# Kernel optimization log

Hardware: AMD Instinct MI355X
Metric: run time of the kernel (lower is better)

The kernel has to match this reference:

```python
import jax, jax.numpy as jnp
import numpy as np

B, DIM, N = 64, 128, 4000
H = 4
DH = DIM // H          # 32
CL = 50                # clusters (hardcoded in module)
K = 9                  # knn_num
SCALOR = DH ** -0.5


def setup_inputs() -> dict:
    key = jax.random.key(0)
    ks = jax.random.split(key, 16)
    s = 0.05
    inp = {
        'x': jax.random.normal(ks[0], (B, DIM, N, 1), jnp.float32),
        # conv_group1 / conv_group2: InstanceNorm(no affine) -> BN(affine) -> ReLU -> 1x1 conv
        'wg1': jax.random.normal(ks[1], (CL, DIM), jnp.float32) * s,
        'bg1': jnp.zeros((CL,), jnp.float32),
        'g1_gamma': jnp.ones((DIM,), jnp.float32),
        'g1_beta': jnp.zeros((DIM,), jnp.float32),
        'wg2': jax.random.normal(ks[2], (CL, DIM), jnp.float32) * s,
        'bg2': jnp.zeros((CL,), jnp.float32),
        'g2_gamma': jnp.ones((DIM,), jnp.float32),
        'g2_beta': jnp.zeros((DIM,), jnp.float32),
        # per-head 1x1 convs (stacked over heads)
        'qkv_w': jax.random.normal(ks[3], (H, DH, DIM), jnp.float32) * s,
        'qkv_b': jnp.zeros((H, DH), jnp.float32),
        'qkv1_w': jax.random.normal(ks[4], (H, 3 * DH, DIM), jnp.float32) * s,
        'qkv1_b': jnp.zeros((H, 3 * DH), jnp.float32),
        # GCBlock convs: conv1 (1,3) stride (1,3): 2*DH->DH ; conv2 (1,3): DH->DH
        'gc1_w': jax.random.normal(ks[5], (H, DH, 2 * DH, 3), jnp.float32) * s,
        'gc1_b': jnp.zeros((H, DH), jnp.float32),
        'gc1_gamma': jnp.ones((H, DH), jnp.float32),
        'gc1_beta': jnp.zeros((H, DH), jnp.float32),
        'gc2_w': jax.random.normal(ks[6], (H, DH, DH, 3), jnp.float32) * s,
        'gc2_b': jnp.zeros((H, DH), jnp.float32),
        'gc2_gamma': jnp.ones((H, DH), jnp.float32),
        'gc2_beta': jnp.zeros((H, DH), jnp.float32),
        # output projections
        'pres_w': jax.random.normal(ks[7], (DIM, 2 * DIM), jnp.float32) * s,
        'pres_b': jnp.zeros((DIM,), jnp.float32),
        'proj_w': jax.random.normal(ks[8], (DIM, DIM), jnp.float32) * s,
        'proj_b': jnp.zeros((DIM,), jnp.float32),
    }
    return inp


def _conv_group(x3, w, bconv, gamma, beta):
    # x3: (b, C, n). InstanceNorm2d(eps=1e-3, no affine) over n, BN(train) over (b,n), ReLU, 1x1 conv.
    mu = x3.mean(-1, keepdims=True)
    var = x3.var(-1, keepdims=True)
    xin = (x3 - mu) * jax.lax.rsqrt(var + 1e-3)
    mu2 = xin.mean((0, 2), keepdims=True)
    var2 = xin.var((0, 2), keepdims=True)
    xbn = gamma[None, :, None] * (xin - mu2) * jax.lax.rsqrt(var2 + 1e-5) + beta[None, :, None]
    xr = jax.nn.relu(xbn)
    return jnp.einsum('oc,bcn->bon', w, xr) + bconv[None, :, None]


def _bn_train(h, gamma, beta, axes):
    mu = h.mean(axes, keepdims=True)
    var = h.var(axes, keepdims=True)
    return gamma * (h - mu) * jax.lax.rsqrt(var + 1e-5) + beta


def _forward(x, wg1, bg1, g1_gamma, g1_beta, wg2, bg2, g2_gamma, g2_beta,
             qkv_w, qkv_b, qkv1_w, qkv1_b,
             gc1_w, gc1_b, gc1_gamma, gc1_beta,
             gc2_w, gc2_b, gc2_gamma, gc2_beta,
             pres_w, pres_b, proj_w, proj_b):
    xs = x[..., 0]                                          # (b, dim, n)
    # cluster assignment 1: softmax over points
    embed1 = _conv_group(xs, wg1, bg1, g1_gamma, g1_beta)   # (b, 50, n)
    S1 = jax.nn.softmax(embed1, axis=2)
    cluster_x = jnp.einsum('bdn,bcn->bdc', xs, S1)          # (b, dim, 50)

    # ---- local branch (per head, vectorized): 1x1 conv -> knn graph feature -> conv stack ----
    q = jnp.einsum('hod,bdc->bhoc', qkv_w, cluster_x) + qkv_b[None, :, :, None]  # (b,H,dh,50)
    xt = q.transpose(0, 1, 3, 2)                            # (b,H,50,dh)
    inner = jnp.einsum('bhnc,bhmc->bhnm', xt, xt)
    sq = jnp.sum(xt * xt, axis=-1)
    pd = 2.0 * inner - sq[..., :, None] - sq[..., None, :]  # negative squared distance
    idx = jax.lax.top_k(pd, K)[1]                            # (b,H,50,K)
    x_exp = jnp.broadcast_to(xt[:, :, None, :, :], xt.shape[:2] + (CL, CL, DH))
    feature = jnp.take_along_axis(x_exp, idx[..., None], axis=3)        # (b,H,50,K,dh)
    center = jnp.broadcast_to(xt[:, :, :, None, :], feature.shape)
    edge = jnp.concatenate([center, center - feature], axis=-1)          # (b,H,50,K,2dh)
    # conv1: kernel (1,3) stride (1,3): K=9 -> 3 windows of 3
    e = edge.reshape(edge.shape[0], H, CL, 3, 3, 2 * DH)
    h1 = jnp.einsum('bhnjti,hoit->bhnjo', e, gc1_w) + gc1_b[None, :, None, None, :]
    h1 = jax.nn.relu(_bn_train(h1, gc1_gamma[None, :, None, None, :], gc1_beta[None, :, None, None, :], (0, 2, 3)))
    # conv2: kernel (1,3): 3 -> 1
    h2 = jnp.einsum('bhnti,hoit->bhno', h1, gc2_w) + gc2_b[None, :, None, :]
    h2 = jax.nn.relu(_bn_train(h2, gc2_gamma[None, :, None, :], gc2_beta[None, :, None, :], (0, 2)))
    local = h2.transpose(0, 1, 3, 2)                        # (b,H,dh,50)

    # ---- global branch: tiny attention over 50 clusters per head ----
    qkv = jnp.einsum('hod,bdc->bhoc', qkv1_w, cluster_x) + qkv1_b[None, :, :, None]  # (b,H,3dh,50)
    qg, kg, vg = jnp.split(qkv, 3, axis=2)
    attn = jax.nn.softmax(SCALOR * jnp.einsum('bhdn,bhdm->bhnm', qg, kg), axis=-1)
    glob = jnp.einsum('bhnm,bhdm->bhdn', attn, vg)          # (b,H,dh,50)

    # interleave [local_h, global_h] per head along channels -> (b, 2*dim, 50)
    per_head = jnp.concatenate([local, glob], axis=2)       # (b,H,2dh,50)
    cat = per_head.reshape(per_head.shape[0], 2 * DIM, CL)
    res = jnp.einsum('oc,bcn->bon', pres_w, cat) + pres_b[None, :, None]  # (b,dim,50)

    # cluster assignment 2: softmax over clusters, scatter back to points
    embed2 = _conv_group(xs, wg2, bg2, g2_gamma, g2_beta)   # (b,50,n)
    S2 = jax.nn.softmax(embed2, axis=1)
    res2 = jnp.einsum('bdc,bcn->bdn', res, S2)              # (b,dim,n)
    out = jnp.einsum('od,bdn->bon', proj_w, res2) + proj_b[None, :, None]
    return out[..., None]                                   # (b,dim,n,1)


def reference(x, wg1, bg1, g1_gamma, g1_beta, wg2, bg2, g2_gamma, g2_beta,
              qkv_w, qkv_b, qkv1_w, qkv1_b,
              gc1_w, gc1_b, gc1_gamma, gc1_beta,
              gc2_w, gc2_b, gc2_gamma, gc2_beta,
              pres_w, pres_b, proj_w, proj_b):
    return _forward(x, wg1, bg1, g1_gamma, g1_beta, wg2, bg2, g2_gamma, g2_beta,
                    qkv_w, qkv_b, qkv1_w, qkv1_b,
                    gc1_w, gc1_b, gc1_gamma, gc1_beta,
                    gc2_w, gc2_b, gc2_gamma, gc2_beta,
                    pres_w, pres_b, proj_w, proj_b)
```

## Files before the change

kernel.cpp:

```cpp
#include <hip/hip_runtime.h>
#include <cstddef>


constexpr size_t O_MU    = 0;
constexpr size_t O_RINV  = 8192;
constexpr size_t O_RATIO = 16384;
constexpr size_t O_A1    = 24576;
constexpr size_t O_B1    = 24704;
constexpr size_t O_A2    = 24832;
constexpr size_t O_B2    = 24960;
constexpr size_t O_PROJWT= 25088;
constexpr size_t O_VPROJ = 41472;
constexpr size_t O_MT    = 41600;
constexpr size_t O_E2    = 74368;
constexpr size_t O_UCXP  = 12874368;
constexpr size_t O_CX    = 16659072;
constexpr size_t O_XT    = 17068672;
constexpr size_t O_QT    = 17478272;
constexpr size_t O_KT    = 17887872;
constexpr size_t O_VT    = 18297472;
constexpr size_t O_H1    = 18707072;
constexpr size_t O_P1    = 19935872;
constexpr size_t O_BN1S  = 19952256;
constexpr size_t O_BN1T  = 19952384;
constexpr size_t O_H2    = 19952512;
constexpr size_t O_P2    = 20362112;
constexpr size_t O_BN2S  = 20378496;
constexpr size_t O_BN2T  = 20378624;
constexpr size_t O_CAT   = 20378752;
constexpr size_t O_PRES2 = 21197952;

__global__ __launch_bounds__(256) void k_rowstats(const float* __restrict__ x,
                                                  float* __restrict__ ws){
  int row = blockIdx.x;
  const float4* xr = (const float4*)(x + (size_t)row * 4000);
  float s = 0.f, sq = 0.f;
  for(int i = threadIdx.x; i < 1000; i += 256){
    float4 v = xr[i];
    s  += v.x + v.y + v.z + v.w;
    sq += v.x*v.x + v.y*v.y + v.z*v.z + v.w*v.w;
  }
  __shared__ float ls[256], lq[256];
  ls[threadIdx.x] = s; lq[threadIdx.x] = sq; __syncthreads();
  for(int st = 128; st > 0; st >>= 1){
    if(threadIdx.x < st){ ls[threadIdx.x] += ls[threadIdx.x+st]; lq[threadIdx.x] += lq[threadIdx.x+st]; }
    __syncthreads();
  }
  if(threadIdx.x == 0){
    float mean = ls[0] * (1.f/4000.f);
    float var  = lq[0] * (1.f/4000.f) - mean*mean;
    ws[O_MU   + row] = mean;
    ws[O_RINV + row] = rsqrtf(var + 1e-3f);
    ws[O_RATIO+ row] = var / (var + 1e-3f);
  }
}

__global__ void k_prep(const float* g1g, const float* g1b,
                       const float* g2g, const float* g2b,
                       const float* presb, const float* projw,
                       float* __restrict__ ws){
  int t = threadIdx.x;
  if(t < 128){
    float s = 0.f;
    for(int b = 0; b < 64; b++) s += ws[O_RATIO + b*128 + t];
    float var2 = s * (1.f/64.f);
    float inv2 = rsqrtf(var2 + 1e-5f);
    ws[O_A1+t] = g1g[t] * inv2;  ws[O_B1+t] = g1b[t];
    ws[O_A2+t] = g2g[t] * inv2;  ws[O_B2+t] = g2b[t];
  }
  for(int i = t; i < 16384; i += 256){ int o = i & 127, k = i >> 7; ws[O_PROJWT+i] = projw[o*128 + k]; }
  __syncthreads();
  if(t < 128){
    float v = 0.f;
    for(int d = 0; d < 128; d++) v += ws[O_PROJWT + d*128 + t] * presb[d];
    ws[O_VPROJ + t] = v;
  }
}

__global__ __launch_bounds__(256) void k_mprep(const float* __restrict__ presw,
                                               float* __restrict__ ws){
  int kk2 = blockIdx.x * 2;
  __shared__ float pwc[2][128];
  int t = threadIdx.x;
  { int which = t >> 7, d = t & 127; pwc[which][d] = presw[d*256 + kk2 + which]; }
  __syncthreads();
  int which = t >> 7, o = t & 127;
  float acc = 0.f;
  for(int d = 0; d < 128; d++) acc += ws[O_PROJWT + d*128 + o] * pwc[which][d];
  ws[O_MT + (size_t)(kk2 + which)*128 + o] = acc;
}

__global__ __launch_bounds__(256) void k_e1ucx(const float* __restrict__ x,
    const float* __restrict__ wg1, const float* __restrict__ bg1,
    float* __restrict__ ws){
  int ch = blockIdx.x, b = blockIdx.y;
  __shared__ float lW1[128*52];
  __shared__ float lrv1[128*48];
  __shared__ float lxt [48*132];
  __shared__ float ca1[128], cb1[128];
  __shared__ float bg1p[56];
  int t = threadIdx.x;
  if(t < 128){
    float mu = ws[O_MU + b*128 + t], ri = ws[O_RINV + b*128 + t];
    float a1 = ws[O_A1+t]*ri;
    ca1[t] = a1; cb1[t] = ws[O_B1+t] - a1*mu;
  }
  if(t < 56) bg1p[t] = (t < 50) ? bg1[t] : 0.f;
  for(int i = t; i < 1664; i += 256){
    int cl = i >> 5, cq = i & 31;
    float4 w = (cl < 50) ? *(const float4*)&wg1[cl*128 + cq*4] : make_float4(0.f,0.f,0.f,0.f);
    int c0 = cq*4;
    lW1[(c0+0)*52+cl] = w.x; lW1[(c0+1)*52+cl] = w.y;
    lW1[(c0+2)*52+cl] = w.z; lW1[(c0+3)*52+cl] = w.w;
  }
  int dg = t & 31, cg = t >> 5;
  float ua[4][8];
  #pragma unroll
  for(int r = 0; r < 4; r++)
    #pragma unroll
    for(int i = 0; i < 8; i++) ua[r][i] = 0.f;
  float zacc = 0.f;
  int ig = t >> 4, jg = t & 15;
  int clb = ig*4, j4 = jg*4;

  for(int st = 0; st < 11; st++){
    int nb = ch*500 + st*48;
    int lim = (st == 10) ? 20 : 48;
    __syncthreads();
    for(int i = t; i < 1536; i += 256){
      int c = i / 12, jj = (i % 12)*4;
      float4 xv = make_float4(0.f,0.f,0.f,0.f);
      if(jj < lim) xv = *(const float4*)&x[(size_t)(b*128 + c)*4000 + nb + jj];
      lxt[(jj+0)*132 + c] = xv.x; lxt[(jj+1)*132 + c] = xv.y;
      lxt[(jj+2)*132 + c] = xv.z; lxt[(jj+3)*132 + c] = xv.w;
      float a1 = ca1[c], b1v = cb1[c];
      float4 r1;
      r1.x = fmaxf(a1*xv.x + b1v, 0.f); r1.y = fmaxf(a1*xv.y + b1v, 0.f);
      r1.z = fmaxf(a1*xv.z + b1v, 0.f); r1.w = fmaxf(a1*xv.w + b1v, 0.f);
      *(float4*)&lrv1[c*48 + jj] = r1;
    }
    __syncthreads();
    float e[4][4];
    if(ig < 13 && jg < 12){
      #pragma unroll
      for(int r = 0; r < 4; r++){ e[r][0]=0.f; e[r][1]=0.f; e[r][2]=0.f; e[r][3]=0.f; }
      #pragma unroll 4
      for(int c = 0; c < 128; c++){
        float4 w = *(const float4*)&lW1[c*52 + clb];
        float4 v = *(const float4*)&lrv1[c*48 + j4];
        e[0][0] += w.x*v.x; e[0][1] += w.x*v.y; e[0][2] += w.x*v.z; e[0][3] += w.x*v.w;
        e[1][0] += w.y*v.x; e[1][1] += w.y*v.y; e[1][2] += w.y*v.z; e[1][3] += w.y*v.w;
        e[2][0] += w.z*v.x; e[2][1] += w.z*v.y; e[2][2] += w.z*v.z; e[2][3] += w.z*v.w;
        e[3][0] += w.w*v.x; e[3][1] += w.w*v.y; e[3][2] += w.w*v.z; e[3][3] += w.w*v.w;
      }
    }
    __syncthreads();
    if(ig < 13 && jg < 12){
      bool live = (j4 < lim);
      #pragma unroll
      for(int r = 0; r < 4; r++){
        float bias = bg1p[clb + r];
        float4 u = make_float4(0.f,0.f,0.f,0.f);
        if(live){
          u.x = expf(e[r][0] + bias); u.y = expf(e[r][1] + bias);
          u.z = expf(e[r][2] + bias); u.w = expf(e[r][3] + bias);
        }
        *(float4*)&lrv1[(clb + r)*48 + j4] = u;
      }
    }
    __syncthreads();
    if(t < 224){
      int d4 = dg*4, c8 = cg*8;
      for(int n4 = 0; n4 < 12; n4++){
        int n0 = n4*4;
        float4 uv[8];
        #pragma unroll
        for(int i = 0; i < 8; i++) uv[i] = *(const float4*)&lrv1[(c8 + i)*48 + n0];
        {
          float4 xq = *(const float4*)&lxt[(n0+0)*132 + d4];
          #pragma unroll
          for(int i = 0; i < 8; i++){
            float u = uv[i].x;
            ua[0][i] += xq.x*u; ua[1][i] += xq.y*u; ua[2][i] += xq.z*u; ua[3][i] += xq.w*u;
          }
        }
        {
          float4 xq = *(const float4*)&lxt[(n0+1)*132 + d4];
          #pragma unroll
          for(int i = 0; i < 8; i++){
            float u = uv[i].y;
            ua[0][i] += xq.x*u; ua[1][i] += xq.y*u; ua[2][i] += xq.z*u; ua[3][i] += xq.w*u;
          }
        }
        {
          float4 xq = *(const float4*)&lxt[(n0+2)*132 + d4];
          #pragma unroll
          for(int i = 0; i < 8; i++){
            float u = uv[i].z;
            ua[0][i] += xq.x*u; ua[1][i] += xq.y*u; ua[2][i] += xq.z*u; ua[3][i] += xq.w*u;
          }
        }
        {
          float4 xq = *(const float4*)&lxt[(n0+3)*132 + d4];
          #pragma unroll
          for(int i = 0; i < 8; i++){
            float u = uv[i].w;
            ua[0][i] += xq.x*u; ua[1][i] += xq.y*u; ua[2][i] += xq.z*u; ua[3][i] += xq.w*u;
          }
        }
      }
    }
    if(t < 52){
      float s = 0.f;
      #pragma unroll
      for(int k = 0; k < 12; k++){
        float4 u = *(const float4*)&lrv1[t*48 + k*4];
        s += u.x + u.y + u.z + u.w;
      }
      zacc += s;
    }
  }
  if(t < 224){
    int d4 = dg*4, c8 = cg*8;
    #pragma unroll
    for(int r = 0; r < 4; r++){
      size_t base = O_UCXP + ((size_t)(ch*64 + b)*132 + d4 + r)*56 + c8;
      *(float4*)&ws[base]     = make_float4(ua[r][0], ua[r][1], ua[r][2], ua[r][3]);
      *(float4*)&ws[base + 4] = make_float4(ua[r][4], ua[r][5], ua[r][6], ua[r][7]);
    }
  }
  if(t < 52) ws[O_UCXP + ((size_t)(ch*64 + b)*132 + 128)*56 + t] = zacc;
}

__global__ __launch_bounds__(256) void k_e2(const float* __restrict__ x,
    const float* __restrict__ wg2, const float* __restrict__ bg2,
    float* __restrict__ ws){
  int ch = blockIdx.x, b = blockIdx.y;
  __shared__ float lW2[128*52];
  __shared__ float lrv2[128*64];
  __shared__ float ca2[128], cb2[128];
  __shared__ float bg2p[56];
  int t = threadIdx.x;
  if(t < 128){
    float mu = ws[O_MU + b*128 + t], ri = ws[O_RINV + b*128 + t];
    float a2 = ws[O_A2+t]*ri;
    ca2[t] = a2; cb2[t] = ws[O_B2+t] - a2*mu;
  }
  if(t < 56) bg2p[t] = (t < 50) ? bg2[t] : 0.f;
  for(int i = t; i < 1664; i += 256){
    int cl = i >> 5, cq = i & 31;
    float4 w = (cl < 50) ? *(const float4*)&wg2[cl*128 + cq*4] : make_float4(0.f,0.f,0.f,0.f);
    int c0 = cq*4;
    lW2[(c0+0)*52+cl] = w.x; lW2[(c0+1)*52+cl] = w.y;
    lW2[(c0+2)*52+cl] = w.z; lW2[(c0+3)*52+cl] = w.w;
  }
  int ig = t >> 4, jg = t & 15;
  int clb = ig*4, j4 = jg*4;
  for(int st = 0; st < 8; st++){
    int nb = ch*500 + st*64;
    int lim = (st == 7) ? 52 : 64;
    __syncthreads();
    for(int i = t; i < 2048; i += 256){
      int c = i >> 4, jj = (i & 15)*4;
      float4 xv = make_float4(0.f,0.f,0.f,0.f);
      if(jj < lim) xv = *(const float4*)&x[(size_t)(b*128 + c)*4000 + nb + jj];
      float a2 = ca2[c], b2v = cb2[c];
      float4 r2;
      r2.x = fmaxf(a2*xv.x + b2v, 0.f); r2.y = fmaxf(a2*xv.y + b2v, 0.f);
      r2.z = fmaxf(a2*xv.z + b2v, 0.f); r2.w = fmaxf(a2*xv.w + b2v, 0.f);
      *(float4*)&lrv2[c*64 + jj] = r2;
    }
    __syncthreads();
    if(ig < 13){
      float e[4][4];
      #pragma unroll
      for(int r = 0; r < 4; r++){ e[r][0]=0.f; e[r][1]=0.f; e[r][2]=0.f; e[r][3]=0.f; }
      #pragma unroll 4
      for(int c = 0; c < 128; c++){
        float4 w = *(const float4*)&lW2[c*52 + clb];
        float4 v = *(const float4*)&lrv2[c*64 + j4];
        e[0][0] += w.x*v.x; e[0][1] += w.x*v.y; e[0][2] += w.x*v.z; e[0][3] += w.x*v.w;
        e[1][0] += w.y*v.x; e[1][1] += w.y*v.y; e[1][2] += w.y*v.z; e[1][3] += w.y*v.w;
        e[2][0] += w.z*v.x; e[2][1] += w.z*v.y; e[2][2] += w.z*v.z; e[2][3] += w.z*v.w;
        e[3][0] += w.w*v.x; e[3][1] += w.w*v.y; e[3][2] += w.w*v.z; e[3][3] += w.w*v.w;
      }
      if(j4 < lim){
        #pragma unroll
        for(int r = 0; r < 4; r++){
          int cl = clb + r;
          if(cl < 50){
            float bias = bg2p[cl];
            float4 o = make_float4(e[r][0]+bias, e[r][1]+bias, e[r][2]+bias, e[r][3]+bias);
            *(float4*)&ws[O_E2 + ((size_t)b*50 + cl)*4000 + nb + j4] = o;
          }
        }
      }
    }
  }
}

__global__ __launch_bounds__(256) void k_cxred(float* __restrict__ ws){
  int b = blockIdx.x, t = threadIdx.x;
  __shared__ float zi[64];
  if(t < 50){
    float s = 0.f;
    for(int ch = 0; ch < 8; ch++)
      s += ws[O_UCXP + ((size_t)(ch*64 + b)*132 + 128)*56 + t];
    zi[t] = 1.f / s;
  }
  __syncthreads();
  for(int i = t; i < 6400; i += 256){
    int d = i / 50, c = i % 50;
    float s = 0.f;
    for(int ch = 0; ch < 8; ch++)
      s += ws[O_UCXP + ((size_t)(ch*64 + b)*132 + d)*56 + c];
    ws[O_CX + (size_t)b*6400 + d*50 + c] = s * zi[c];
  }
}

__global__ __launch_bounds__(256) void k_qkv(const float* __restrict__ qw,
                                             const float* __restrict__ qb,
                                             const float* __restrict__ q1w,
                                             const float* __restrict__ q1b,
                                             float* __restrict__ ws){
  int rt = blockIdx.x, b = blockIdx.y;
  __shared__ float wl[64*130];
  __shared__ float cxl[128*52];
  int t = threadIdx.x;
  for(int i = t; i < 2048; i += 256){
    int rl = i >> 5, kq = i & 31, row = rt*64 + rl;
    float4 w = (row < 128) ? *(const float4*)&qw[row*128 + kq*4]
                           : *(const float4*)&q1w[(row-128)*128 + kq*4];
    int k0 = kq*4;
    wl[rl*130 + k0+0] = w.x; wl[rl*130 + k0+1] = w.y;
    wl[rl*130 + k0+2] = w.z; wl[rl*130 + k0+3] = w.w;
  }
  for(int i = t; i < 6656; i += 256){
    int k = i / 52, c = i % 52;
    cxl[i] = (c < 50) ? ws[O_CX + (size_t)b*6400 + k*50 + c] : 0.f;
  }
  __syncthreads();
  int ig = t & 15, cg = t >> 4;
  float acc[4][4];
  #pragma unroll
  for(int r = 0; r < 4; r++){ acc[r][0]=0.f; acc[r][1]=0.f; acc[r][2]=0.f; acc[r][3]=0.f; }
  if(cg < 13){
    int rb = ig*4, cb = cg*4;
    #pragma unroll 4
    for(int k = 0; k < 128; k++){
      float4 cv = *(const float4*)&cxl[k*52 + cb];
      float w0 = wl[(rb+0)*130 + k], w1 = wl[(rb+1)*130 + k];
      float w2 = wl[(rb+2)*130 + k], w3 = wl[(rb+3)*130 + k];
      acc[0][0] += w0*cv.x; acc[0][1] += w0*cv.y; acc[0][2] += w0*cv.z; acc[0][3] += w0*cv.w;
      acc[1][0] += w1*cv.x; acc[1][1] += w1*cv.y; acc[1][2] += w1*cv.z; acc[1][3] += w1*cv.w;
      acc[2][0] += w2*cv.x; acc[2][1] += w2*cv.y; acc[2][2] += w2*cv.z; acc[2][3] += w2*cv.w;
      acc[3][0] += w3*cv.x; acc[3][1] += w3*cv.y; acc[3][2] += w3*cv.z; acc[3][3] += w3*cv.w;
    }
    #pragma unroll
    for(int r = 0; r < 4; r++){
      int row = rt*64 + ig*4 + r;
      size_t base; float bias;
      if(row < 128){
        int h = row >> 5;
        bias = qb[row];
        base = O_XT + (size_t)(b*4 + h)*1600 + (row & 31);
      }else{
        int r2 = row - 128, h = r2/96, j = r2%96, kind = j >> 5, dd = j & 31;
        bias = q1b[r2];
        base = (kind==0 ? O_QT : kind==1 ? O_KT : O_VT) + (size_t)(b*4 + h)*1600 + dd;
      }
      #pragma unroll
      for(int s = 0; s < 4; s++){
        int c = cg*4 + s;
        if(c < 50) ws[base + (size_t)c*32] = acc[r][s] + bias;
      }
    }
  }
}

__global__ __launch_bounds__(256) void k_knn(const float* __restrict__ g1w,
                                             const float* __restrict__ g1bias,
                                             float* __restrict__ ws){
  int h = blockIdx.x, b = blockIdx.y;
  __shared__ float xtl[50][33];
  __shared__ float pdl[50][52];
  __shared__ float sql[50];
  __shared__ int   idxl[50][9];
  __shared__ float w1l[6144];
  int t = threadIdx.x;
  const float* xtg = ws + O_XT + (size_t)(b*4 + h)*1600;
  for(int i = t; i < 1600; i += 256) xtl[i >> 5][i & 31] = xtg[i];
  for(int i = t; i < 6144; i += 256){
    int o = i / 192, r = i % 192, ii = r / 3, tt = r % 3;
    w1l[(ii*3 + tt)*32 + o] = g1w[(size_t)h*6144 + i];
  }
  __syncthreads();
  if(t < 50){
    float s = 0.f;
    for(int d = 0; d < 32; d++){ float v = xtl[t][d]; s += v*v; }
    sql[t] = s;
  }
  __syncthreads();
  for(int i = t; i < 2500; i += 256){
    int n = i / 50, m = i % 50;
    float s = 0.f;
    for(int d = 0; d < 32; d++) s += xtl[n][d]*xtl[m][d];
    pdl[n][m] = 2.f*s - sql[n] - sql[m];
  }
  __syncthreads();
  if(t < 50){
    float pv = INFINITY; int pi = -1;
    for(int k = 0; k < 9; k++){
      float bv = -INFINITY; int bi = 1000;
      for(int m = 0; m < 50; m++){
        float v = pdl[t][m];
        bool elig = (v < pv) || (v == pv && m > pi);
        if(elig && (v > bv || (v == bv && m < bi))){ bv = v; bi = m; }
      }
      idxl[t][k] = bi; pv = bv; pi = bi;
    }
  }
  __syncthreads();
  if(t < 150){
    int n = t / 3, jw = t % 3;
    float acc[32];
    #pragma unroll
    for(int o = 0; o < 32; o++) acc[o] = 0.f;
    for(int t3 = 0; t3 < 3; t3++){
      int kx = idxl[n][jw*3 + t3];
      for(int ii = 0; ii < 32; ii++){
        float c0 = xtl[n][ii];
        float c1 = c0 - xtl[kx][ii];
        const float* wr0 = w1l + (ii*3 + t3)*32;
        const float* wr1 = w1l + ((ii+32)*3 + t3)*32;
        #pragma unroll
        for(int o = 0; o < 32; o++) acc[o] += c0*wr0[o] + c1*wr1[o];
      }
    }
    float* out = ws + O_H1 + ((size_t)(b*4 + h)*150 + n*3 + jw)*32;
    #pragma unroll
    for(int o = 0; o < 32; o++) out[o] = acc[o] + g1bias[h*32 + o];
  }
}

__global__ void k_bn1p(float* __restrict__ ws){
  int b = blockIdx.x, t = threadIdx.x;
  int p = t & 127, half = t >> 7;
  int h = p >> 5, o = p & 31;
  const float* src = ws + O_H1 + (size_t)b*19200;
  float s = 0.f, sq = 0.f;
  for(int nj = half*75; nj < half*75 + 75; nj++){
    float v = src[(h*150 + nj)*32 + o];
    s += v; sq += v*v;
  }
  __shared__ float ls[256], lq[256];
  ls[t] = s; lq[t] = sq; __syncthreads();
  if(t < 128){
    ws[O_P1 + b*256 + p]       = ls[t] + ls[t+128];
    ws[O_P1 + b*256 + 128 + p] = lq[t] + lq[t+128];
  }
}

__global__ void k_bn1f(const float* g, const float* be, float* __restrict__ ws){
  int t = threadIdx.x;
  if(t < 128){
    float s = 0.f, sq = 0.f;
    for(int b = 0; b < 64; b++){ s += ws[O_P1 + b*256 + t]; sq += ws[O_P1 + b*256 + 128 + t]; }
    float mean = s * (1.f/9600.f), var = sq * (1.f/9600.f) - mean*mean;
    float sc = g[t] * rsqrtf(var + 1e-5f);
    ws[O_BN1S+t] = sc; ws[O_BN1T+t] = be[t] - sc*mean;
  }
}

__global__ __launch_bounds__(256) void k_conv2(const float* __restrict__ g2w,
                                               const float* __restrict__ g2bias,
                                               float* __restrict__ ws){
  int h = blockIdx.x, b = blockIdx.y;
  __shared__ float hl[150][33];
  __shared__ float w2l[3072];
  __shared__ float rs[8][32], rq[8][32];
  int t = threadIdx.x;
  const float* h1p = ws + O_H1 + (size_t)(b*4 + h)*4800;
  for(int i = t; i < 4800; i += 256){
    int nj = i >> 5, ii = i & 31;
    hl[nj][ii] = fmaxf(ws[O_BN1S + h*32 + ii]*h1p[i] + ws[O_BN1T + h*32 + ii], 0.f);
  }
  for(int i = t; i < 3072; i += 256){
    int o = i / 96, r = i % 96, ii = r / 3, tt = r % 3;
    w2l[(ii*3 + tt)*32 + o] = g2w[(size_t)h*3072 + i];
  }
  __syncthreads();
  int o = t & 31, ng = t >> 5;
  float bias = g2bias[h*32 + o];
  float s = 0.f, sq = 0.f;
  for(int n = ng; n < 50; n += 8){
    float acc = 0.f;
    for(int t3 = 0; t3 < 3; t3++){
      const float* hr = hl[n*3 + t3];
      #pragma unroll
      for(int ii = 0; ii < 32; ii++) acc += hr[ii] * w2l[(ii*3 + t3)*32 + o];
    }
    acc += bias;
    ws[O_H2 + ((size_t)(b*4 + h)*50 + n)*32 + o] = acc;
    s += acc; sq += acc*acc;
  }
  rs[ng][o] = s; rq[ng][o] = sq; __syncthreads();
  if(t < 32){
    float S = 0.f, Q = 0.f;
    for(int g2 = 0; g2 < 8; g2++){ S += rs[g2][t]; Q += rq[g2][t]; }
    ws[O_P2 + (b*4 + h)*64 + t]      = S;
    ws[O_P2 + (b*4 + h)*64 + 32 + t] = Q;
  }
}

__global__ void k_bn2f(const float* g, const float* be, float* __restrict__ ws){
  int t = threadIdx.x;
  if(t < 128){
    int h = t >> 5, o = t & 31;
    float s = 0.f, sq = 0.f;
    for(int b = 0; b < 64; b++){
      s  += ws[O_P2 + (size_t)(b*4 + h)*64 + o];
      sq += ws[O_P2 + (size_t)(b*4 + h)*64 + 32 + o];
    }
    float mean = s * (1.f/3200.f), var = sq * (1.f/3200.f) - mean*mean;
    float sc = g[t] * rsqrtf(var + 1e-5f);
    ws[O_BN2S+t] = sc; ws[O_BN2T+t] = be[t] - sc*mean;
  }
}

__global__ __launch_bounds__(256) void k_attn(float* __restrict__ ws){
  int h = blockIdx.x, b = blockIdx.y;
  __shared__ float qtl[50][33], ktl[50][33], vtl[50][33], al[50][52];
  int t = threadIdx.x;
  size_t base = (size_t)(b*4 + h)*1600;
  for(int i = t; i < 1600; i += 256){
    int n = i >> 5, d = i & 31;
    qtl[n][d] = ws[O_QT + base + i];
    ktl[n][d] = ws[O_KT + base + i];
    vtl[n][d] = ws[O_VT + base + i];
  }
  __syncthreads();
  for(int i = t; i < 2500; i += 256){
    int n = i / 50, m = i % 50;
    float s = 0.f;
    for(int d = 0; d < 32; d++) s += qtl[n][d]*ktl[m][d];
    al[n][m] = s * 0.17677669529663687f;
  }
  __syncthreads();
  if(t < 50){
    float m = -INFINITY;
    for(int j = 0; j < 50; j++) m = fmaxf(m, al[t][j]);
    float s = 0.f;
    for(int j = 0; j < 50; j++){ float e = expf(al[t][j] - m); al[t][j] = e; s += e; }
    float inv = 1.f/s;
    for(int j = 0; j < 50; j++) al[t][j] *= inv;
  }
  __syncthreads();
  for(int i = t; i < 1600; i += 256){
    int n = i >> 5, d = i & 31;
    float gacc = 0.f;
    for(int m = 0; m < 50; m++) gacc += al[n][m]*vtl[m][d];
    ws[O_CAT + ((size_t)b*256 + h*64 + 32 + d)*50 + n] = gacc;
    float l = fmaxf(ws[O_BN2S + h*32 + d]*ws[O_H2 + ((size_t)(b*4 + h)*50 + n)*32 + d] + ws[O_BN2T + h*32 + d], 0.f);
    ws[O_CAT + ((size_t)b*256 + h*64 + d)*50 + n] = l;
  }
}

__global__ __launch_bounds__(256) void k_res(float* __restrict__ ws){
  int b = blockIdx.x;
  __shared__ float mtl[64*132];
  __shared__ float catl[64*52];
  __shared__ float vp[128];
  int t = threadIdx.x;
  if(t < 128) vp[t] = ws[O_VPROJ + t];
  int og = t >> 4, cg = t & 15;
  int ob = og*8, cb = cg*4;
  float acc[8][4];
  #pragma unroll
  for(int r = 0; r < 8; r++){ acc[r][0]=0.f; acc[r][1]=0.f; acc[r][2]=0.f; acc[r][3]=0.f; }
  for(int kc = 0; kc < 4; kc++){
    int k0 = kc*64;
    __syncthreads();
    for(int i = t; i < 2048; i += 256){
      int k = i >> 5, oq = i & 31;
      float4 m = *(const float4*)&ws[O_MT + (size_t)(k0 + k)*128 + oq*4];
      *(float4*)&mtl[k*132 + oq*4] = m;
    }
    for(int i = t; i < 3328; i += 256){
      int k = i / 52, c = i % 52;
      catl[i] = (c < 50) ? ws[O_CAT + (size_t)b*12800 + (k0 + k)*50 + c] : 0.f;
    }
    __syncthreads();
    if(cg < 13){
      #pragma unroll 2
      for(int k = 0; k < 64; k++){
        float4 m0 = *(const float4*)&mtl[k*132 + ob];
        float4 m1 = *(const float4*)&mtl[k*132 + ob + 4];
        float4 cv = *(const float4*)&catl[k*52 + cb];
        acc[0][0] += m0.x*cv.x; acc[0][1] += m0.x*cv.y; acc[0][2] += m0.x*cv.z; acc[0][3] += m0.x*cv.w;
        acc[1][0] += m0.y*cv.x; acc[1][1] += m0.y*cv.y; acc[1][2] += m0.y*cv.z; acc[1][3] += m0.y*cv.w;
        acc[2][0] += m0.z*cv.x; acc[2][1] += m0.z*cv.y; acc[2][2] += m0.z*cv.z; acc[2][3] += m0.z*cv.w;
        acc[3][0] += m0.w*cv.x; acc[3][1] += m0.w*cv.y; acc[3][2] += m0.w*cv.z; acc[3][3] += m0.w*cv.w;
        acc[4][0] += m1.x*cv.x; acc[4][1] += m1.x*cv.y; acc[4][2] += m1.x*cv.z; acc[4][3] += m1.x*cv.w;
        acc[5][0] += m1.y*cv.x; acc[5][1] += m1.y*cv.y; acc[5][2] += m1.y*cv.z; acc[5][3] += m1.y*cv.w;
        acc[6][0] += m1.z*cv.x; acc[6][1] += m1.z*cv.y; acc[6][2] += m1.z*cv.z; acc[6][3] += m1.z*cv.w;
        acc[7][0] += m1.w*cv.x; acc[7][1] += m1.w*cv.y; acc[7][2] += m1.w*cv.z; acc[7][3] += m1.w*cv.w;
      }
    }
  }
  if(cg < 13){
    #pragma unroll
    for(int s = 0; s < 4; s++){
      int c = cb + s;
      if(c < 50){
        float4 o0 = make_float4(acc[0][s]+vp[ob+0], acc[1][s]+vp[ob+1], acc[2][s]+vp[ob+2], acc[3][s]+vp[ob+3]);
        float4 o1 = make_float4(acc[4][s]+vp[ob+4], acc[5][s]+vp[ob+5], acc[6][s]+vp[ob+6], acc[7][s]+vp[ob+7]);
        *(float4*)&ws[O_PRES2 + (size_t)b*6400 + c*128 + ob]     = o0;
        *(float4*)&ws[O_PRES2 + (size_t)b*6400 + c*128 + ob + 4] = o1;
      }
    }
  }
}

__global__ __launch_bounds__(256) void k_out(const float* __restrict__ projb,
                                             float* __restrict__ ws,
                                             float* __restrict__ out){
  int nt = blockIdx.x, b = blockIdx.y;
  int n0 = nt*64;
  __shared__ float sl[50*64];
  __shared__ float p2l[50*132];
  __shared__ float pb[128];
  int t = threadIdx.x;
  for(int i = t; i < 3200; i += 256){
    int c = i >> 6, j = i & 63, n = n0 + j;
    sl[i] = (n < 4000) ? ws[O_E2 + ((size_t)b*50 + c)*4000 + n] : 0.f;
  }
  for(int i = t; i < 6400; i += 256){
    int c = i >> 7, o = i & 127;
    p2l[c*132 + o] = ws[O_PRES2 + (size_t)b*6400 + c*128 + o];
  }
  if(t < 128) pb[t] = projb[t];
  __syncthreads();
  if(t < 64){
    int j = t;
    float m = -INFINITY;
    for(int c = 0; c < 50; c++) m = fmaxf(m, sl[c*64 + j]);
    float s = 0.f;
    for(int c = 0; c < 50; c++){ float e = expf(sl[c*64 + j] - m); sl[c*64 + j] = e; s += e; }
    float inv = 1.f/s;
    for(int c = 0; c < 50; c++) sl[c*64 + j] *= inv;
  }
  __syncthreads();
  int og = t >> 4, jg = t & 15;
  int ob = og*8, j4 = jg*4;
  float acc[8][4];
  #pragma unroll
  for(int r = 0; r < 8; r++){ acc[r][0]=0.f; acc[r][1]=0.f; acc[r][2]=0.f; acc[r][3]=0.f; }
  #pragma unroll 2
  for(int c = 0; c < 50; c++){
    float4 sv = *(const float4*)&sl[c*64 + j4];
    float4 p0 = *(const float4*)&p2l[c*132 + ob];
    float4 p1 = *(const float4*)&p2l[c*132 + ob + 4];
    acc[0][0] += p0.x*sv.x; acc[0][1] += p0.x*sv.y; acc[0][2] += p0.x*sv.z; acc[0][3] += p0.x*sv.w;
    acc[1][0] += p0.y*sv.x; acc[1][1] += p0.y*sv.y; acc[1][2] += p0.y*sv.z; acc[1][3] += p0.y*sv.w;
    acc[2][0] += p0.z*sv.x; acc[2][1] += p0.z*sv.y; acc[2][2] += p0.z*sv.z; acc[2][3] += p0.z*sv.w;
    acc[3][0] += p0.w*sv.x; acc[3][1] += p0.w*sv.y; acc[3][2] += p0.w*sv.z; acc[3][3] += p0.w*sv.w;
    acc[4][0] += p1.x*sv.x; acc[4][1] += p1.x*sv.y; acc[4][2] += p1.x*sv.z; acc[4][3] += p1.x*sv.w;
    acc[5][0] += p1.y*sv.x; acc[5][1] += p1.y*sv.y; acc[5][2] += p1.y*sv.z; acc[5][3] += p1.y*sv.w;
    acc[6][0] += p1.z*sv.x; acc[6][1] += p1.z*sv.y; acc[6][2] += p1.z*sv.z; acc[6][3] += p1.z*sv.w;
    acc[7][0] += p1.w*sv.x; acc[7][1] += p1.w*sv.y; acc[7][2] += p1.w*sv.z; acc[7][3] += p1.w*sv.w;
  }
  int n = n0 + j4;
  if(n < 4000){
    #pragma unroll
    for(int r = 0; r < 8; r++){
      float bv = pb[ob + r];
      float4 o = make_float4(acc[r][0]+bv, acc[r][1]+bv, acc[r][2]+bv, acc[r][3]+bv);
      *(float4*)&out[(size_t)(b*128 + ob + r)*4000 + n] = o;
    }
  }
}

extern "C" void kernel_launch(void* const* d_in, const int* in_sizes, int n_in,
                              void* d_out, int out_size, void* d_ws, size_t ws_size,
                              hipStream_t stream){
  (void)in_sizes; (void)n_in; (void)out_size; (void)ws_size;
  const float* x      = (const float*)d_in[0];
  const float* wg1    = (const float*)d_in[1];
  const float* bg1    = (const float*)d_in[2];
  const float* g1g    = (const float*)d_in[3];
  const float* g1b    = (const float*)d_in[4];
  const float* wg2    = (const float*)d_in[5];
  const float* bg2    = (const float*)d_in[6];
  const float* g2g    = (const float*)d_in[7];
  const float* g2b    = (const float*)d_in[8];
  const float* qkvw   = (const float*)d_in[9];
  const float* qkvb   = (const float*)d_in[10];
  const float* qkv1w  = (const float*)d_in[11];
  const float* qkv1b  = (const float*)d_in[12];
  const float* gc1w   = (const float*)d_in[13];
  const float* gc1bias= (const float*)d_in[14];
  const float* gc1g   = (const float*)d_in[15];
  const float* gc1be  = (const float*)d_in[16];
  const float* gc2w   = (const float*)d_in[17];
  const float* gc2bias= (const float*)d_in[18];
  const float* gc2g   = (const float*)d_in[19];
  const float* gc2be  = (const float*)d_in[20];
  const float* presw  = (const float*)d_in[21];
  const float* presb  = (const float*)d_in[22];
  const float* projw  = (const float*)d_in[23];
  const float* projb  = (const float*)d_in[24];
  float* ws = (float*)d_ws;
  float* out = (float*)d_out;

  k_rowstats<<<8192, 256, 0, stream>>>(x, ws);
  k_prep<<<1, 256, 0, stream>>>(g1g, g1b, g2g, g2b, presb, projw, ws);
  k_mprep<<<128, 256, 0, stream>>>(presw, ws);
  k_e1ucx<<<dim3(8, 64), 256, 0, stream>>>(x, wg1, bg1, ws);
  k_e2<<<dim3(8, 64), 256, 0, stream>>>(x, wg2, bg2, ws);
  k_cxred<<<64, 256, 0, stream>>>(ws);
  k_qkv<<<dim3(8, 64), 256, 0, stream>>>(qkvw, qkvb, qkv1w, qkv1b, ws);
  k_knn<<<dim3(4, 64), 256, 0, stream>>>(gc1w, gc1bias, ws);
  k_bn1p<<<64, 256, 0, stream>>>(ws);
  k_bn1f<<<1, 128, 0, stream>>>(gc1g, gc1be, ws);
  k_conv2<<<dim3(4, 64), 256, 0, stream>>>(gc2w, gc2bias, ws);
  k_bn2f<<<1, 128, 0, stream>>>(gc2g, gc2be, ws);
  k_attn<<<dim3(4, 64), 256, 0, stream>>>(ws);
  k_res<<<64, 256, 0, stream>>>(ws);
  k_out<<<dim3(63, 64), 256, 0, stream>>>(projb, ws, out);
}
```

Before: 796.8 us.

## Fuse small reduction kernels, add register prefetch, and use wave-shuffle row stats

```diff
diff --git a/kernel.cpp b/kernel.cpp
--- a/kernel.cpp
+++ b/kernel.cpp
@@ -14,53 +14,48 @@
 constexpr size_t O_MT    = 41600;
 constexpr size_t O_E2    = 74368;
 constexpr size_t O_UCXP  = 12874368;
-constexpr size_t O_CX    = 16659072;
 constexpr size_t O_XT    = 17068672;
 constexpr size_t O_QT    = 17478272;
 constexpr size_t O_KT    = 17887872;
 constexpr size_t O_VT    = 18297472;
 constexpr size_t O_H1    = 18707072;
 constexpr size_t O_P1    = 19935872;
-constexpr size_t O_BN1S  = 19952256;
-constexpr size_t O_BN1T  = 19952384;
 constexpr size_t O_H2    = 19952512;
 constexpr size_t O_P2    = 20362112;
-constexpr size_t O_BN2S  = 20378496;
-constexpr size_t O_BN2T  = 20378624;
 constexpr size_t O_CAT   = 20378752;
 constexpr size_t O_PRES2 = 21197952;
 
 __global__ __launch_bounds__(256) void k_rowstats(const float* __restrict__ x,
                                                   float* __restrict__ ws){
-  int row = blockIdx.x;
+  int w = threadIdx.x >> 6, lane = threadIdx.x & 63;
+  int row = blockIdx.x*4 + w;
   const float4* xr = (const float4*)(x + (size_t)row * 4000);
   float s = 0.f, sq = 0.f;
-  for(int i = threadIdx.x; i < 1000; i += 256){
+  for(int i = lane; i < 1000; i += 64){
     float4 v = xr[i];
     s  += v.x + v.y + v.z + v.w;
     sq += v.x*v.x + v.y*v.y + v.z*v.z + v.w*v.w;
   }
-  __shared__ float ls[256], lq[256];
-  ls[threadIdx.x] = s; lq[threadIdx.x] = sq; __syncthreads();
-  for(int st = 128; st > 0; st >>= 1){
-    if(threadIdx.x < st){ ls[threadIdx.x] += ls[threadIdx.x+st]; lq[threadIdx.x] += lq[threadIdx.x+st]; }
-    __syncthreads();
-  }
-  if(threadIdx.x == 0){
-    float mean = ls[0] * (1.f/4000.f);
-    float var  = lq[0] * (1.f/4000.f) - mean*mean;
+  for(int off = 32; off > 0; off >>= 1){
+    s  += __shfl_down(s,  off, 64);
+    sq += __shfl_down(sq, off, 64);
+  }
+  if(lane == 0){
+    float mean = s * (1.f/4000.f);
+    float var  = sq * (1.f/4000.f) - mean*mean;
     ws[O_MU   + row] = mean;
     ws[O_RINV + row] = rsqrtf(var + 1e-3f);
     ws[O_RATIO+ row] = var / (var + 1e-3f);
   }
 }
 
-__global__ void k_prep(const float* g1g, const float* g1b,
+__global__ __launch_bounds__(256) void k_prep(const float* g1g, const float* g1b,
                        const float* g2g, const float* g2b,
-                       const float* presb, const float* projw,
-                       float* __restrict__ ws){
-  int t = threadIdx.x;
-  if(t < 128){
+                       const float* projw, float* __restrict__ ws){
+  int t = threadIdx.x;
+  int i = blockIdx.x*256 + t;
+  { int o = i & 127, k = i >> 7; ws[O_PROJWT+i] = projw[o*128 + k]; }
+  if(blockIdx.x == 0 && t < 128){
     float s = 0.f;
     for(int b = 0; b < 64; b++) s += ws[O_RATIO + b*128 + t];
     float var2 = s * (1.f/64.f);
@@ -68,26 +63,28 @@
     ws[O_A1+t] = g1g[t] * inv2;  ws[O_B1+t] = g1b[t];
     ws[O_A2+t] = g2g[t] * inv2;  ws[O_B2+t] = g2b[t];
   }
-  for(int i = t; i < 16384; i += 256){ int o = i & 127, k = i >> 7; ws[O_PROJWT+i] = projw[o*128 + k]; }
-  __syncthreads();
-  if(t < 128){
-    float v = 0.f;
-    for(int d = 0; d < 128; d++) v += ws[O_PROJWT + d*128 + t] * presb[d];
-    ws[O_VPROJ + t] = v;
-  }
 }
 
 __global__ __launch_bounds__(256) void k_mprep(const float* __restrict__ presw,
+                                               const float* __restrict__ presb,
                                                float* __restrict__ ws){
-  int kk2 = blockIdx.x * 2;
-  __shared__ float pwc[2][128];
-  int t = threadIdx.x;
-  { int which = t >> 7, d = t & 127; pwc[which][d] = presw[d*256 + kk2 + which]; }
-  __syncthreads();
-  int which = t >> 7, o = t & 127;
-  float acc = 0.f;
-  for(int d = 0; d < 128; d++) acc += ws[O_PROJWT + d*128 + o] * pwc[which][d];
-  ws[O_MT + (size_t)(kk2 + which)*128 + o] = acc;
+  int t = threadIdx.x;
+  if(blockIdx.x < 128){
+    int kk2 = blockIdx.x * 2;
+    __shared__ float pwc[2][128];
+    { int which = t >> 7, d = t & 127; pwc[which][d] = presw[d*256 + kk2 + which]; }
+    __syncthreads();
+    int which = t >> 7, o = t & 127;
+    float acc = 0.f;
+    for(int d = 0; d < 128; d++) acc += ws[O_PROJWT + d*128 + o] * pwc[which][d];
+    ws[O_MT + (size_t)(kk2 + which)*128 + o] = acc;
+  }else{
+    if(t < 128){
+      float v = 0.f;
+      for(int d = 0; d < 128; d++) v += ws[O_PROJWT + d*128 + t] * presb[d];
+      ws[O_VPROJ + t] = v;
+    }
+  }
 }
 
 __global__ __launch_bounds__(256) void k_e1ucx(const float* __restrict__ x,
@@ -122,15 +119,21 @@
   float zacc = 0.f;
   int ig = t >> 4, jg = t & 15;
   int clb = ig*4, j4 = jg*4;
+  int sc[6], sj[6];
+  float4 pf[6];
+  #pragma unroll
+  for(int j = 0; j < 6; j++){ int i = t + 256*j; sc[j] = i/12; sj[j] = (i%12)*4; }
+  #pragma unroll
+  for(int j = 0; j < 6; j++)
+    pf[j] = *(const float4*)&x[(size_t)(b*128 + sc[j])*4000 + ch*500 + sj[j]];
 
   for(int st = 0; st < 11; st++){
-    int nb = ch*500 + st*48;
     int lim = (st == 10) ? 20 : 48;
     __syncthreads();
-    for(int i = t; i < 1536; i += 256){
-      int c = i / 12, jj = (i % 12)*4;
-      float4 xv = make_float4(0.f,0.f,0.f,0.f);
-      if(jj < lim) xv = *(const float4*)&x[(size_t)(b*128 + c)*4000 + nb + jj];
+    #pragma unroll
+    for(int j = 0; j < 6; j++){
+      int c = sc[j], jj = sj[j];
+      float4 xv = (jj < lim) ? pf[j] : make_float4(0.f,0.f,0.f,0.f);
       lxt[(jj+0)*132 + c] = xv.x; lxt[(jj+1)*132 + c] = xv.y;
       lxt[(jj+2)*132 + c] = xv.z; lxt[(jj+3)*132 + c] = xv.w;
       float a1 = ca1[c], b1v = cb1[c];
@@ -140,6 +143,14 @@
       *(float4*)&lrv1[c*48 + jj] = r1;
     }
     __syncthreads();
+    if(st < 10){
+      int lim2 = (st == 9) ? 20 : 48;
+      int nb2 = ch*500 + (st+1)*48;
+      #pragma unroll
+      for(int j = 0; j < 6; j++)
+        pf[j] = (sj[j] < lim2) ? *(const float4*)&x[(size_t)(b*128 + sc[j])*4000 + nb2 + sj[j]]
+                               : make_float4(0.f,0.f,0.f,0.f);
+    }
     float e[4][4];
     if(ig < 13 && jg < 12){
       #pragma unroll
@@ -237,7 +248,7 @@
     float* __restrict__ ws){
   int ch = blockIdx.x, b = blockIdx.y;
   __shared__ float lW2[128*52];
-  __shared__ float lrv2[128*64];
+  __shared__ float lrv2[128*48];
   __shared__ float ca2[128], cb2[128];
   __shared__ float bg2p[56];
   int t = threadIdx.x;
@@ -256,29 +267,45 @@
   }
   int ig = t >> 4, jg = t & 15;
   int clb = ig*4, j4 = jg*4;
-  for(int st = 0; st < 8; st++){
-    int nb = ch*500 + st*64;
-    int lim = (st == 7) ? 52 : 64;
-    __syncthreads();
-    for(int i = t; i < 2048; i += 256){
-      int c = i >> 4, jj = (i & 15)*4;
-      float4 xv = make_float4(0.f,0.f,0.f,0.f);
-      if(jj < lim) xv = *(const float4*)&x[(size_t)(b*128 + c)*4000 + nb + jj];
+  int sc[6], sj[6];
+  float4 pf[6];
+  #pragma unroll
+  for(int j = 0; j < 6; j++){ int i = t + 256*j; sc[j] = i/12; sj[j] = (i%12)*4; }
+  #pragma unroll
+  for(int j = 0; j < 6; j++)
+    pf[j] = *(const float4*)&x[(size_t)(b*128 + sc[j])*4000 + ch*500 + sj[j]];
+
+  for(int st = 0; st < 11; st++){
+    int nb = ch*500 + st*48;
+    int lim = (st == 10) ? 20 : 48;
+    __syncthreads();
+    #pragma unroll
+    for(int j = 0; j < 6; j++){
+      int c = sc[j], jj = sj[j];
+      float4 xv = (jj < lim) ? pf[j] : make_float4(0.f,0.f,0.f,0.f);
       float a2 = ca2[c], b2v = cb2[c];
       float4 r2;
       r2.x = fmaxf(a2*xv.x + b2v, 0.f); r2.y = fmaxf(a2*xv.y + b2v, 0.f);
       r2.z = fmaxf(a2*xv.z + b2v, 0.f); r2.w = fmaxf(a2*xv.w + b2v, 0.f);
-      *(float4*)&lrv2[c*64 + jj] = r2;
-    }
-    __syncthreads();
-    if(ig < 13){
+      *(float4*)&lrv2[c*48 + jj] = r2;
+    }
+    __syncthreads();
+    if(st < 10){
+      int lim2 = (st == 9) ? 20 : 48;
+      int nb2 = ch*500 + (st+1)*48;
+      #pragma unroll
+      for(int j = 0; j < 6; j++)
+        pf[j] = (sj[j] < lim2) ? *(const float4*)&x[(size_t)(b*128 + sc[j])*4000 + nb2 + sj[j]]
+                               : make_float4(0.f,0.f,0.f,0.f);
+    }
+    if(ig < 13 && jg < 12){
       float e[4][4];
       #pragma unroll
       for(int r = 0; r < 4; r++){ e[r][0]=0.f; e[r][1]=0.f; e[r][2]=0.f; e[r][3]=0.f; }
       #pragma unroll 4
       for(int c = 0; c < 128; c++){
         float4 w = *(const float4*)&lW2[c*52 + clb];
-        float4 v = *(const float4*)&lrv2[c*64 + j4];
+        float4 v = *(const float4*)&lrv2[c*48 + j4];
         e[0][0] += w.x*v.x; e[0][1] += w.x*v.y; e[0][2] += w.x*v.z; e[0][3] += w.x*v.w;
         e[1][0] += w.y*v.x; e[1][1] += w.y*v.y; e[1][2] += w.y*v.z; e[1][3] += w.y*v.w;
         e[2][0] += w.z*v.x; e[2][1] += w.z*v.y; e[2][2] += w.z*v.z; e[2][3] += w.z*v.w;
@@ -299,25 +326,6 @@
   }
 }
 
-__global__ __launch_bounds__(256) void k_cxred(float* __restrict__ ws){
-  int b = blockIdx.x, t = threadIdx.x;
-  __shared__ float zi[64];
-  if(t < 50){
-    float s = 0.f;
-    for(int ch = 0; ch < 8; ch++)
-      s += ws[O_UCXP + ((size_t)(ch*64 + b)*132 + 128)*56 + t];
-    zi[t] = 1.f / s;
-  }
-  __syncthreads();
-  for(int i = t; i < 6400; i += 256){
-    int d = i / 50, c = i % 50;
-    float s = 0.f;
-    for(int ch = 0; ch < 8; ch++)
-      s += ws[O_UCXP + ((size_t)(ch*64 + b)*132 + d)*56 + c];
-    ws[O_CX + (size_t)b*6400 + d*50 + c] = s * zi[c];
-  }
-}
-
 __global__ __launch_bounds__(256) void k_qkv(const float* __restrict__ qw,
                                              const float* __restrict__ qb,
                                              const float* __restrict__ q1w,
@@ -326,7 +334,17 @@
   int rt = blockIdx.x, b = blockIdx.y;
   __shared__ float wl[64*130];
   __shared__ float cxl[128*52];
-  int t = threadIdx.x;
+  __shared__ float zi[52];
+  int t = threadIdx.x;
+  if(t < 52){
+    float s = 0.f;
+    if(t < 50){
+      #pragma unroll
+      for(int ch = 0; ch < 8; ch++)
+        s += ws[O_UCXP + ((size_t)(ch*64 + b)*132 + 128)*56 + t];
+      zi[t] = 1.f / s;
+    }else zi[t] = 0.f;
+  }
   for(int i = t; i < 2048; i += 256){
     int rl = i >> 5, kq = i & 31, row = rt*64 + rl;
     float4 w = (row < 128) ? *(const float4*)&qw[row*128 + kq*4]
@@ -335,9 +353,14 @@
     wl[rl*130 + k0+0] = w.x; wl[rl*130 + k0+1] = w.y;
     wl[rl*130 + k0+2] = w.z; wl[rl*130 + k0+3] = w.w;
   }
+  __syncthreads();
   for(int i = t; i < 6656; i += 256){
     int k = i / 52, c = i % 52;
-    cxl[i] = (c < 50) ? ws[O_CX + (size_t)b*6400 + k*50 + c] : 0.f;
+    float s = 0.f;
+    size_t base = O_UCXP + ((size_t)b*132 + k)*56 + c;
+    #pragma unroll
+    for(int ch = 0; ch < 8; ch++) s += ws[base + (size_t)ch*64*132*56];
+    cxl[i] = s * zi[c];
   }
   __syncthreads();
   int ig = t & 15, cg = t >> 4;
@@ -443,51 +466,55 @@
   }
 }
 
-__global__ void k_bn1p(float* __restrict__ ws){
-  int b = blockIdx.x, t = threadIdx.x;
-  int p = t & 127, half = t >> 7;
-  int h = p >> 5, o = p & 31;
-  const float* src = ws + O_H1 + (size_t)b*19200;
+__global__ __launch_bounds__(256) void k_bn1p(float* __restrict__ ws){
+  int h = blockIdx.x, b = blockIdx.y, t = threadIdx.x;
+  int o = t & 31, part = t >> 5;
+  const float* src = ws + O_H1 + (size_t)(b*4 + h)*4800;
   float s = 0.f, sq = 0.f;
-  for(int nj = half*75; nj < half*75 + 75; nj++){
-    float v = src[(h*150 + nj)*32 + o];
+  for(int nj = part; nj < 150; nj += 8){
+    float v = src[nj*32 + o];
     s += v; sq += v*v;
   }
-  __shared__ float ls[256], lq[256];
-  ls[t] = s; lq[t] = sq; __syncthreads();
-  if(t < 128){
-    ws[O_P1 + b*256 + p]       = ls[t] + ls[t+128];
-    ws[O_P1 + b*256 + 128 + p] = lq[t] + lq[t+128];
-  }
-}
-
-__global__ void k_bn1f(const float* g, const float* be, float* __restrict__ ws){
-  int t = threadIdx.x;
-  if(t < 128){
-    float s = 0.f, sq = 0.f;
-    for(int b = 0; b < 64; b++){ s += ws[O_P1 + b*256 + t]; sq += ws[O_P1 + b*256 + 128 + t]; }
-    float mean = s * (1.f/9600.f), var = sq * (1.f/9600.f) - mean*mean;
-    float sc = g[t] * rsqrtf(var + 1e-5f);
-    ws[O_BN1S+t] = sc; ws[O_BN1T+t] = be[t] - sc*mean;
-  }
-}
-
-__global__ __launch_bounds__(256) void k_conv2(const float* __restrict__ g2w,
+  __shared__ float rs[8][33], rq[8][33];
+  rs[part][o] = s; rq[part][o] = sq; __syncthreads();
+  if(t < 32){
+    float S = 0.f, Q = 0.f;
+    for(int p = 0; p < 8; p++){ S += rs[p][t]; Q += rq[p][t]; }
+    ws[O_P1 + b*256 + h*32 + t]       = S;
+    ws[O_P1 + b*256 + 128 + h*32 + t] = Q;
+  }
+}
+
+__global__ __launch_bounds__(256) void k_conv2(const float* __restrict__ g1g,
+                                               const float* __restrict__ g1be,
+                                               const float* __restrict__ g2w,
                                                const float* __restrict__ g2bias,
                                                float* __restrict__ ws){
   int h = blockIdx.x, b = blockIdx.y;
   __shared__ float hl[150][33];
   __shared__ float w2l[3072];
   __shared__ float rs[8][32], rq[8][32];
-  int t = threadIdx.x;
+  __shared__ float b1s[32], b1t[32];
+  int t = threadIdx.x;
+  if(t < 32){
+    float s = 0.f, sq = 0.f;
+    for(int bb = 0; bb < 64; bb++){
+      s  += ws[O_P1 + bb*256 + h*32 + t];
+      sq += ws[O_P1 + bb*256 + 128 + h*32 + t];
+    }
+    float mean = s * (1.f/9600.f), var = sq * (1.f/9600.f) - mean*mean;
+    float sc = g1g[h*32+t] * rsqrtf(var + 1e-5f);
+    b1s[t] = sc; b1t[t] = g1be[h*32+t] - sc*mean;
+  }
+  for(int i = t; i < 3072; i += 256){
+    int o = i / 96, r = i % 96, ii = r / 3, tt = r % 3;
+    w2l[(ii*3 + tt)*32 + o] = g2w[(size_t)h*3072 + i];
+  }
+  __syncthreads();
   const float* h1p = ws + O_H1 + (size_t)(b*4 + h)*4800;
   for(int i = t; i < 4800; i += 256){
     int nj = i >> 5, ii = i & 31;
-    hl[nj][ii] = fmaxf(ws[O_BN1S + h*32 + ii]*h1p[i] + ws[O_BN1T + h*32 + ii], 0.f);
-  }
-  for(int i = t; i < 3072; i += 256){
-    int o = i / 96, r = i % 96, ii = r / 3, tt = r % 3;
-    w2l[(ii*3 + tt)*32 + o] = g2w[(size_t)h*3072 + i];
+    hl[nj][ii] = fmaxf(b1s[ii]*h1p[i] + b1t[ii], 0.f);
   }
   __syncthreads();
   int o = t & 31, ng = t >> 5;
@@ -513,25 +540,23 @@
   }
 }
 
-__global__ void k_bn2f(const float* g, const float* be, float* __restrict__ ws){
-  int t = threadIdx.x;
-  if(t < 128){
-    int h = t >> 5, o = t & 31;
-    float s = 0.f, sq = 0.f;
-    for(int b = 0; b < 64; b++){
-      s  += ws[O_P2 + (size_t)(b*4 + h)*64 + o];
-      sq += ws[O_P2 + (size_t)(b*4 + h)*64 + 32 + o];
-    }
-    float mean = s * (1.f/3200.f), var = sq * (1.f/3200.f) - mean*mean;
-    float sc = g[t] * rsqrtf(var + 1e-5f);
-    ws[O_BN2S+t] = sc; ws[O_BN2T+t] = be[t] - sc*mean;
-  }
-}
-
-__global__ __launch_bounds__(256) void k_attn(float* __restrict__ ws){
+__global__ __launch_bounds__(256) void k_attn(const float* __restrict__ g2g,
+                                              const float* __restrict__ g2be,
+                                              float* __restrict__ ws){
   int h = blockIdx.x, b = blockIdx.y;
   __shared__ float qtl[50][33], ktl[50][33], vtl[50][33], al[50][52];
-  int t = threadIdx.x;
+  __shared__ float b2s[32], b2t[32];
+  int t = threadIdx.x;
+  if(t < 32){
+    float s = 0.f, sq = 0.f;
+    for(int bb = 0; bb < 64; bb++){
+      s  += ws[O_P2 + (size_t)(bb*4 + h)*64 + t];
+      sq += ws[O_P2 + (size_t)(bb*4 + h)*64 + 32 + t];
+    }
+    float mean = s * (1.f/3200.f), var = sq * (1.f/3200.f) - mean*mean;
+    float sc = g2g[h*32+t] * rsqrtf(var + 1e-5f);
+    b2s[t] = sc; b2t[t] = g2be[h*32+t] - sc*mean;
+  }
   size_t base = (size_t)(b*4 + h)*1600;
   for(int i = t; i < 1600; i += 256){
     int n = i >> 5, d = i & 31;
@@ -561,7 +586,7 @@
     float gacc = 0.f;
     for(int m = 0; m < 50; m++) gacc += al[n][m]*vtl[m][d];
     ws[O_CAT + ((size_t)b*256 + h*64 + 32 + d)*50 + n] = gacc;
-    float l = fmaxf(ws[O_BN2S + h*32 + d]*ws[O_H2 + ((size_t)(b*4 + h)*50 + n)*32 + d] + ws[O_BN2T + h*32 + d], 0.f);
+    float l = fmaxf(b2s[d]*ws[O_H2 + ((size_t)(b*4 + h)*50 + n)*32 + d] + b2t[d], 0.f);
     ws[O_CAT + ((size_t)b*256 + h*64 + d)*50 + n] = l;
   }
 }
@@ -713,19 +738,16 @@
   float* ws = (float*)d_ws;
   float* out = (float*)d_out;
 
-  k_rowstats<<<8192, 256, 0, stream>>>(x, ws);
-  k_prep<<<1, 256, 0, stream>>>(g1g, g1b, g2g, g2b, presb, projw, ws);
-  k_mprep<<<128, 256, 0, stream>>>(presw, ws);
+  k_rowstats<<<2048, 256, 0, stream>>>(x, ws);
+  k_prep<<<64, 256, 0, stream>>>(g1g, g1b, g2g, g2b, projw, ws);
+  k_mprep<<<129, 256, 0, stream>>>(presw, presb, ws);
   k_e1ucx<<<dim3(8, 64), 256, 0, stream>>>(x, wg1, bg1, ws);
   k_e2<<<dim3(8, 64), 256, 0, stream>>>(x, wg2, bg2, ws);
-  k_cxred<<<64, 256, 0, stream>>>(ws);
   k_qkv<<<dim3(8, 64), 256, 0, stream>>>(qkvw, qkvb, qkv1w, qkv1b, ws);
   k_knn<<<dim3(4, 64), 256, 0, stream>>>(gc1w, gc1bias, ws);
-  k_bn1p<<<64, 256, 0, stream>>>(ws);
-  k_bn1f<<<1, 128, 0, stream>>>(gc1g, gc1be, ws);
-  k_conv2<<<dim3(4, 64), 256, 0, stream>>>(gc2w, gc2bias, ws);
-  k_bn2f<<<1, 128, 0, stream>>>(gc2g, gc2be, ws);
-  k_attn<<<dim3(4, 64), 256, 0, stream>>>(ws);
+  k_bn1p<<<dim3(4, 64), 256, 0, stream>>>(ws);
+  k_conv2<<<dim3(4, 64), 256, 0, stream>>>(gc1g, gc1be, gc2w, gc2bias, ws);
+  k_attn<<<dim3(4, 64), 256, 0, stream>>>(gc2g, gc2be, ws);
   k_res<<<64, 256, 0, stream>>>(ws);
   k_out<<<dim3(63, 64), 256, 0, stream>>>(projb, ws, out);
 }
```

New measurement: 779.3 us. 1.02x faster.
